# Kernel tuning notes

Measured on AMD Instinct MI355X. Metric: run time of the kernel, lower is better.

Reference implementation:

```python
import jax, jax.numpy as jnp
import numpy as np

M, OUT, IN = 512, 8192, 8192
BLOCK_N, BLOCK_K = 128, 128  # weight_block_size (out_block, in_block)
OB, IB = OUT // BLOCK_N, IN // BLOCK_K  # 64, 64 scale blocks


def setup_inputs() -> dict:
    key = jax.random.key(0)
    k1, k2, k3 = jax.random.split(key, 3)
    x = jax.random.normal(k1, (M, IN), dtype=jnp.float32)
    # pre-quantized int8 weight stored as (out_features, in_features)
    weight_q = jax.random.randint(k2, (OUT, IN), -127, 127, dtype=jnp.int32).astype(jnp.int8)
    # per-(out_block, in_block) dequant scales
    weight_scale = jax.random.uniform(k3, (OB, IB), dtype=jnp.float32, minval=0.01, maxval=0.02)
    return {"x": x, "weight_q": weight_q, "weight_scale": weight_scale}


def _dequant(weight_q, weight_scale):
    # (OUT, IN) int8 -> blocks (OB, BLOCK_N, IB, BLOCK_K), scale broadcast per block
    w = weight_q.astype(jnp.float32).reshape(OB, BLOCK_N, IB, BLOCK_K)
    w = w * weight_scale[:, None, :, None]
    return w.reshape(OUT, IN)


def reference(x, weight_q, weight_scale):
    # Block-dequantize then matmul: out[m, o] = sum_i x[m, i] * (wq[o, i] * scale[o//bn, i//bk])
    w = _dequant(weight_q, weight_scale)          # (OUT, IN) fp32
    out = jnp.einsum("mi,oi->mo", x, w)           # (M, OUT)
    return out
```

## Files before the change

kernel.cpp:

```cpp
#include <hip/hip_runtime.h>

#define MDIM 512
#define NDIM 8192
#define KDIM 8192

typedef float v4f __attribute__((ext_vector_type(4)));
typedef int   v4i __attribute__((ext_vector_type(4)));
typedef char  c16 __attribute__((ext_vector_type(16)));

#define GLDS16(g, l)                                                    \
  __builtin_amdgcn_global_load_lds(                                     \
      (const __attribute__((address_space(1))) void*)(g),               \
      (__attribute__((address_space(3))) void*)(l), 16, 0, 0)
#define SB __builtin_amdgcn_sched_barrier(0)

__device__ __forceinline__ int swb(int row, int g) {
  return ((row >> 1) << 7) + (((((row & 1) << 2) | g) ^ ((row >> 1) & 7)) << 4);
}

__global__ __launch_bounds__(256) void produce_kernel(
    const int* __restrict__ wq, const float* __restrict__ x,
    char* __restrict__ w8, char* __restrict__ xq, float* __restrict__ ax) {
  if (blockIdx.x < 16384) {
    const int tid = blockIdx.x * 256 + threadIdx.x;
    const int R = tid >> 9;
    const int k16 = tid & 511;
    const int* src = wq + ((size_t)R << 13) + k16 * 16;
    v4i a[4];
#pragma unroll
    for (int h = 0; h < 4; ++h) a[h] = *(const v4i*)(src + h * 4);
    c16 q;
#pragma unroll
    for (int h = 0; h < 4; ++h) {
      q[h * 4 + 0] = (char)a[h][0];
      q[h * 4 + 1] = (char)a[h][1];
      q[h * 4 + 2] = (char)a[h][2];
      q[h * 4 + 3] = (char)a[h][3];
    }
    const int ntile = R >> 6, r = R & 63;
    const int kt = k16 >> 2, g = k16 & 3;
    *(c16*)(w8 + ((size_t)(ntile * 128 + kt) << 12) + swb(r, g)) = q;
  } else {
    const int m = blockIdx.x - 16384;
    const int t = threadIdx.x;
    const float* row = x + ((size_t)m << 13);
    v4f v[8];
    float mx = 0.f;
#pragma unroll
    for (int i = 0; i < 8; ++i) {
      v[i] = *(const v4f*)(row + t * 32 + i * 4);
#pragma unroll
      for (int r = 0; r < 4; ++r) mx = fmaxf(mx, fabsf(v[i][r]));
    }
#pragma unroll
    for (int d = 1; d < 64; d <<= 1) mx = fmaxf(mx, __shfl_xor(mx, d));
    __shared__ float smx[4];
    if ((t & 63) == 0) smx[t >> 6] = mx;
    __syncthreads();
    mx = fmaxf(fmaxf(smx[0], smx[1]), fmaxf(smx[2], smx[3]));
    const float inv = (mx > 0.f) ? 127.f / mx : 0.f;
    if (t == 0) ax[m] = mx / 127.f;
    const int mt = m >> 6, r = m & 63;
#pragma unroll
    for (int g2 = 0; g2 < 2; ++g2) {
      c16 q;
#pragma unroll
      for (int e = 0; e < 16; ++e) {
        const int idx = g2 * 4 + (e >> 2);
        float f = fminf(fmaxf(v[idx][e & 3] * inv, -127.f), 127.f);
        q[e] = (char)__float2int_rn(f);
      }
      const int k16 = t * 2 + g2;
      const int kt = k16 >> 2, g = k16 & 3;
      *(c16*)(xq + ((size_t)(mt * 128 + kt) << 12) + swb(r, g)) = q;
    }
  }
}

template <int KS>
__global__ __launch_bounds__(256) void reduce_kernel(const float* __restrict__ p,
                                                     float* __restrict__ out) {
  const size_t i = ((size_t)blockIdx.x * 256 + threadIdx.x) * 4;
  v4f a = *(const v4f*)(p + i);
#pragma unroll
  for (int s = 1; s < KS; ++s) a += *(const v4f*)(p + (size_t)s * MDIM * NDIM + i);
  *(v4f*)(out + i) = a;
}

template <int KS>
__global__ __launch_bounds__(256, 2) void gemm_i8_kernel(
    const char* __restrict__ xq, const char* __restrict__ w8,
    const float* __restrict__ wsc, const float* __restrict__ ax,
    float* __restrict__ outp) {
  constexpr int NPH = 64 / KS;
  __shared__ char lA[2][16384];
  __shared__ char lB[2][16384];

  const int b = blockIdx.x;
  const int c = b & 7;
  const int s = b >> 3;
  const int mt = s & 3;
  const int kh = (KS > 1) ? ((s >> 2) & (KS - 1)) : 0;
  const int nt2 = c * 8 + ((KS > 1) ? (s >> 3) : (s >> 2));
  const int ktg0 = kh * (128 / KS);

  const int t = threadIdx.x;
  const int w = t >> 6, l = t & 63;
  const int wm = (w >> 1) * 64;
  const int wn = (w & 1) * 64;
  const int l15 = l & 15, q = l >> 4;

  v4i acc[4][4] = {};
  v4f facc[4][4] = {};

  auto issue = [&](int tt) {
    const int buf = tt & 1;
#pragma unroll
    for (int it = 0; it < 8; ++it) {
      const int uu = w * 8 + it;
      const int side = uu >> 4;
      const int h = (uu >> 3) & 1;
      const int kt = (uu >> 2) & 1;
      const int qt = uu & 3;
      const int ktile = ktg0 + tt * 2 + kt;
      const char* src =
          (side == 0)
              ? xq + ((size_t)((mt * 2 + h) * 128 + ktile) << 12)
              : w8 + ((size_t)((nt2 * 2 + h) * 128 + ktile) << 12);
      src += qt * 1024 + (size_t)l * 16;
      char* dst = (side == 0) ? &lA[buf][h * 8192 + kt * 4096 + qt * 1024]
                              : &lB[buf][h * 8192 + kt * 4096 + qt * 1024];
      GLDS16(src, dst);
    }
  };

  issue(0);
#pragma unroll 1
  for (int tt = 0; tt < NPH; ++tt) {
    const int cur = tt & 1;
    SB;
    __builtin_amdgcn_s_barrier();
    SB;
    if (tt + 1 < NPH) issue(tt + 1);
    SB;
    if (tt + 1 < NPH)
      asm volatile("s_waitcnt vmcnt(8)" ::: "memory");
    else
      asm volatile("s_waitcnt vmcnt(0)" ::: "memory");
    SB;
    __builtin_amdgcn_s_barrier();
    SB;

#pragma unroll
    for (int kk = 0; kk < 2; ++kk) {
      v4i af[4], bq[4];
#pragma unroll
      for (int i = 0; i < 4; ++i) {
        const int ra = wm + i * 16 + l15;
        af[i] = *(const v4i*)&lA[cur][(ra >> 6) * 8192 + kk * 4096 +
                                      swb(ra & 63, q)];
      }
#pragma unroll
      for (int j = 0; j < 4; ++j) {
        const int rb = wn + j * 16 + l15;
        bq[j] = *(const v4i*)&lB[cur][(rb >> 6) * 8192 + kk * 4096 +
                                      swb(rb & 63, q)];
      }
#pragma unroll
      for (int i = 0; i < 4; ++i)
#pragma unroll
        for (int j = 0; j < 4; ++j)
          acc[i][j] = __builtin_amdgcn_mfma_i32_16x16x64_i8(
              af[i], bq[j], acc[i][j], 0, 0, 0);
    }

    const float sc = wsc[nt2 * 64 + (ktg0 >> 1) + tt];
#pragma unroll
    for (int i = 0; i < 4; ++i)
#pragma unroll
      for (int j = 0; j < 4; ++j) {
#pragma unroll
        for (int r = 0; r < 4; ++r)
          facc[i][j][r] = fmaf(sc, (float)acc[i][j][r], facc[i][j][r]);
        acc[i][j] = v4i{0, 0, 0, 0};
      }
  }

  float* dst = outp + ((KS > 1) ? (size_t)kh * MDIM * NDIM : 0);
#pragma unroll
  for (int i = 0; i < 4; ++i) {
    const int mrow = mt * 128 + wm + i * 16 + q * 4;
#pragma unroll
    for (int j = 0; j < 4; ++j) {
      const int ocol = nt2 * 128 + wn + j * 16 + l15;
#pragma unroll
      for (int r = 0; r < 4; ++r)
        dst[(size_t)(mrow + r) * NDIM + ocol] = ax[mrow + r] * facc[i][j][r];
    }
  }
}

extern "C" void kernel_launch(void* const* d_in, const int* in_sizes, int n_in,
                              void* d_out, int out_size, void* d_ws,
                              size_t ws_size, hipStream_t stream) {
  const float* x = (const float*)d_in[0];
  const int* wq = (const int*)d_in[1];
  const float* wsc = (const float*)d_in[2];
  float* out = (float*)d_out;

  const size_t W8 = (size_t)NDIM * KDIM;
  const size_t XQ = (size_t)MDIM * KDIM;
  const size_t AX = 65536;
  const size_t PS = (size_t)MDIM * NDIM * 4;

  char* w8 = (char*)d_ws;
  char* xq = (char*)d_ws + W8;
  float* ax = (float*)((char*)d_ws + W8 + XQ);
  float* part = (float*)((char*)d_ws + W8 + XQ + AX);

  produce_kernel<<<dim3(16384 + MDIM), dim3(256), 0, stream>>>(wq, x, w8, xq, ax);

  if (ws_size >= W8 + XQ + AX + 2 * PS) {
    gemm_i8_kernel<2><<<dim3(512), dim3(256), 0, stream>>>(xq, w8, wsc, ax, part);
    reduce_kernel<2><<<dim3((MDIM * NDIM) / (256 * 4)), dim3(256), 0, stream>>>(part, out);
  } else {
    gemm_i8_kernel<1><<<dim3(256), dim3(256), 0, stream>>>(xq, w8, wsc, ax, out);
  }
}
```

Measured before the change: 127.7 us.

## Use 512-thread 256x128 GEMM tiles with triple-buffered LDS and split staging

The int8 GEMM now runs 512-thread blocks, each computing a 256x128 output tile. This halves the block count and reuses each staged weight tile across more rows. A three-deep LDS ring of 48 KB stages is refilled in two halves interleaved with each k-subtile's fragment reads, and MFMA sections are raised with s_setprio. The aim is to hide global-to-LDS latency better and cut per-tile weight traffic, at the cost of one block per CU, 144 KB of LDS and an extra barrier per k-tile.

Result: slower. 132.6 us (+3.9%).

```diff
diff --git a/kernel.cpp b/kernel.cpp
--- a/kernel.cpp
+++ b/kernel.cpp
@@ -88,21 +88,20 @@
 }
 
 template <int KS>
-__global__ __launch_bounds__(256, 2) void gemm_i8_kernel(
+__global__ __launch_bounds__(512, 1) void gemm_i8_kernel(
     const char* __restrict__ xq, const char* __restrict__ w8,
     const float* __restrict__ wsc, const float* __restrict__ ax,
     float* __restrict__ outp) {
-  constexpr int NPH = 64 / KS;
-  __shared__ char lA[2][16384];
-  __shared__ char lB[2][16384];
+  constexpr int NKT = 64 / KS;
+  __shared__ char lds[3][49152];
 
   const int b = blockIdx.x;
   const int c = b & 7;
   const int s = b >> 3;
-  const int mt = s & 3;
-  const int kh = (KS > 1) ? ((s >> 2) & (KS - 1)) : 0;
-  const int nt2 = c * 8 + ((KS > 1) ? (s >> 3) : (s >> 2));
-  const int ktg0 = kh * (128 / KS);
+  const int mt = s & 1;
+  const int kh = (s >> 1) & (KS - 1);
+  const int nt = c * 8 + s / (2 * KS);
+  const int k64b = kh * (NKT * 2);
 
   const int t = threadIdx.x;
   const int w = t >> 6, l = t & 63;
@@ -113,68 +112,98 @@
   v4i acc[4][4] = {};
   v4f facc[4][4] = {};
 
-  auto issue = [&](int tt) {
-    const int buf = tt & 1;
-#pragma unroll
-    for (int it = 0; it < 8; ++it) {
-      const int uu = w * 8 + it;
-      const int side = uu >> 4;
-      const int h = (uu >> 3) & 1;
-      const int kt = (uu >> 2) & 1;
-      const int qt = uu & 3;
-      const int ktile = ktg0 + tt * 2 + kt;
-      const char* src =
-          (side == 0)
-              ? xq + ((size_t)((mt * 2 + h) * 128 + ktile) << 12)
-              : w8 + ((size_t)((nt2 * 2 + h) * 128 + ktile) << 12);
-      src += qt * 1024 + (size_t)l * 16;
-      char* dst = (side == 0) ? &lA[buf][h * 8192 + kt * 4096 + qt * 1024]
-                              : &lB[buf][h * 8192 + kt * 4096 + qt * 1024];
-      GLDS16(src, dst);
+  auto stage_half = [&](int t2, int tb, int h) {
+#pragma unroll
+    for (int j = 0; j < 3; ++j) {
+      const int u = h * 24 + w * 3 + j;
+      if (u < 32) {
+        const int sub = u >> 2, qt = u & 3;
+        const int rb = sub >> 1, kt = sub & 1;
+        const char* src =
+            xq + ((size_t)((mt * 4 + rb) * 128 + k64b + t2 * 2 + kt) << 12) +
+            qt * 1024 + (size_t)l * 16;
+        GLDS16(src, &lds[tb][(rb * 2 + kt) * 4096 + qt * 1024]);
+      } else {
+        const int v = u - 32;
+        const int sub = v >> 2, qt = v & 3;
+        const int rb = sub >> 1, kt = sub & 1;
+        const char* src =
+            w8 + ((size_t)((nt * 2 + rb) * 128 + k64b + t2 * 2 + kt) << 12) +
+            qt * 1024 + (size_t)l * 16;
+        GLDS16(src, &lds[tb][32768 + (rb * 2 + kt) * 4096 + qt * 1024]);
+      }
     }
   };
 
-  issue(0);
+  auto read_frags = [&](int cur, int kt, v4i (&af)[4], v4i (&bq)[4]) {
+#pragma unroll
+    for (int i = 0; i < 4; ++i) {
+      const int ra = wm + i * 16 + l15;
+      af[i] = *(const v4i*)&lds[cur][((ra >> 6) * 2 + kt) * 4096 +
+                                     swb(ra & 63, q)];
+    }
+#pragma unroll
+    for (int j = 0; j < 4; ++j) {
+      const int rb = wn + j * 16 + l15;
+      bq[j] = *(const v4i*)&lds[cur][32768 + ((rb >> 6) * 2 + kt) * 4096 +
+                                     swb(rb & 63, q)];
+    }
+  };
+
+  stage_half(0, 0, 0);
+  stage_half(0, 0, 1);
+  stage_half(1, 1, 0);
+  stage_half(1, 1, 1);
+
 #pragma unroll 1
-  for (int tt = 0; tt < NPH; ++tt) {
-    const int cur = tt & 1;
-    SB;
-    __builtin_amdgcn_s_barrier();
-    SB;
-    if (tt + 1 < NPH) issue(tt + 1);
-    SB;
-    if (tt + 1 < NPH)
-      asm volatile("s_waitcnt vmcnt(8)" ::: "memory");
+  for (int tt = 0; tt < NKT; ++tt) {
+    const int cur = tt % 3;
+    const int tgt = (tt + 2) % 3;
+
+    SB;
+    if (tt + 1 < NKT)
+      asm volatile("s_waitcnt vmcnt(6)" ::: "memory");
     else
       asm volatile("s_waitcnt vmcnt(0)" ::: "memory");
     SB;
     __builtin_amdgcn_s_barrier();
     SB;
-
-#pragma unroll
-    for (int kk = 0; kk < 2; ++kk) {
+    {
       v4i af[4], bq[4];
-#pragma unroll
-      for (int i = 0; i < 4; ++i) {
-        const int ra = wm + i * 16 + l15;
-        af[i] = *(const v4i*)&lA[cur][(ra >> 6) * 8192 + kk * 4096 +
-                                      swb(ra & 63, q)];
-      }
-#pragma unroll
-      for (int j = 0; j < 4; ++j) {
-        const int rb = wn + j * 16 + l15;
-        bq[j] = *(const v4i*)&lB[cur][(rb >> 6) * 8192 + kk * 4096 +
-                                      swb(rb & 63, q)];
-      }
+      read_frags(cur, 0, af, bq);
+      if (tt + 2 < NKT) stage_half(tt + 2, tgt, 0);
+      asm volatile("s_waitcnt lgkmcnt(0)" ::: "memory");
+      SB;
+      __builtin_amdgcn_s_setprio(1);
 #pragma unroll
       for (int i = 0; i < 4; ++i)
 #pragma unroll
         for (int j = 0; j < 4; ++j)
-          acc[i][j] = __builtin_amdgcn_mfma_i32_16x16x64_i8(
-              af[i], bq[j], acc[i][j], 0, 0, 0);
-    }
-
-    const float sc = wsc[nt2 * 64 + (ktg0 >> 1) + tt];
+          acc[i][j] = __builtin_amdgcn_mfma_i32_16x16x64_i8(af[i], bq[j],
+                                                            acc[i][j], 0, 0, 0);
+      __builtin_amdgcn_s_setprio(0);
+    }
+
+    SB;
+    __builtin_amdgcn_s_barrier();
+    SB;
+    {
+      v4i af[4], bq[4];
+      read_frags(cur, 1, af, bq);
+      if (tt + 2 < NKT) stage_half(tt + 2, tgt, 1);
+      asm volatile("s_waitcnt lgkmcnt(0)" ::: "memory");
+      SB;
+      __builtin_amdgcn_s_setprio(1);
+#pragma unroll
+      for (int i = 0; i < 4; ++i)
+#pragma unroll
+        for (int j = 0; j < 4; ++j)
+          acc[i][j] = __builtin_amdgcn_mfma_i32_16x16x64_i8(af[i], bq[j],
+                                                            acc[i][j], 0, 0, 0);
+      __builtin_amdgcn_s_setprio(0);
+    }
+
+    const float sc = wsc[nt * 64 + kh * NKT + tt];
 #pragma unroll
     for (int i = 0; i < 4; ++i)
 #pragma unroll
@@ -189,10 +218,10 @@
   float* dst = outp + ((KS > 1) ? (size_t)kh * MDIM * NDIM : 0);
 #pragma unroll
   for (int i = 0; i < 4; ++i) {
-    const int mrow = mt * 128 + wm + i * 16 + q * 4;
+    const int mrow = mt * 256 + wm + i * 16 + q * 4;
 #pragma unroll
     for (int j = 0; j < 4; ++j) {
-      const int ocol = nt2 * 128 + wn + j * 16 + l15;
+      const int ocol = nt * 128 + wn + j * 16 + l15;
 #pragma unroll
       for (int r = 0; r < 4; ++r)
         dst[(size_t)(mrow + r) * NDIM + ocol] = ax[mrow + r] * facc[i][j][r];
@@ -221,9 +250,9 @@
   produce_kernel<<<dim3(16384 + MDIM), dim3(256), 0, stream>>>(wq, x, w8, xq, ax);
 
   if (ws_size >= W8 + XQ + AX + 2 * PS) {
-    gemm_i8_kernel<2><<<dim3(512), dim3(256), 0, stream>>>(xq, w8, wsc, ax, part);
+    gemm_i8_kernel<2><<<dim3(256), dim3(512), 0, stream>>>(xq, w8, wsc, ax, part);
     reduce_kernel<2><<<dim3((MDIM * NDIM) / (256 * 4)), dim3(256), 0, stream>>>(part, out);
   } else {
-    gemm_i8_kernel<1><<<dim3(256), dim3(256), 0, stream>>>(xq, w8, wsc, ax, out);
-  }
-}
+    gemm_i8_kernel<1><<<dim3(128), dim3(512), 0, stream>>>(xq, w8, wsc, ax, out);
+  }
+}
```

## Replace split-K GEMM plus reduce with single-pass 128x64 tile kernel

Applied to the files above, without the earlier changes.

Removes the split-K partial buffers and the separate reduction kernel, so each block computes a 128x64 output tile over the full K range using two waves. This avoids writing and re-reading two full fp32 partial outputs and one kernel launch. In exchange each block has a narrower N tile with less B reuse per A load and fewer waves per block to hide latency.

Measured after the change: 180.7 us. 41.5% more time.

```diff
diff --git a/kernel.cpp b/kernel.cpp
--- a/kernel.cpp
+++ b/kernel.cpp
@@ -77,37 +77,24 @@
   }
 }
 
-template <int KS>
-__global__ __launch_bounds__(256) void reduce_kernel(const float* __restrict__ p,
-                                                     float* __restrict__ out) {
-  const size_t i = ((size_t)blockIdx.x * 256 + threadIdx.x) * 4;
-  v4f a = *(const v4f*)(p + i);
-#pragma unroll
-  for (int s = 1; s < KS; ++s) a += *(const v4f*)(p + (size_t)s * MDIM * NDIM + i);
-  *(v4f*)(out + i) = a;
-}
-
-template <int KS>
-__global__ __launch_bounds__(256, 2) void gemm_i8_kernel(
+__global__ __launch_bounds__(128) void gemm_i8_kernel(
     const char* __restrict__ xq, const char* __restrict__ w8,
     const float* __restrict__ wsc, const float* __restrict__ ax,
-    float* __restrict__ outp) {
-  constexpr int NPH = 64 / KS;
+    float* __restrict__ out) {
+  constexpr int NPH = 64;
   __shared__ char lA[2][16384];
-  __shared__ char lB[2][16384];
+  __shared__ char lB[2][8192];
 
   const int b = blockIdx.x;
   const int c = b & 7;
   const int s = b >> 3;
   const int mt = s & 3;
-  const int kh = (KS > 1) ? ((s >> 2) & (KS - 1)) : 0;
-  const int nt2 = c * 8 + ((KS > 1) ? (s >> 3) : (s >> 2));
-  const int ktg0 = kh * (128 / KS);
+  const int nt = c * 16 + (s >> 2);
+  const int m0 = mt * 128, n0 = nt * 64;
 
   const int t = threadIdx.x;
   const int w = t >> 6, l = t & 63;
-  const int wm = (w >> 1) * 64;
-  const int wn = (w & 1) * 64;
+  const int wm = w * 64;
   const int l15 = l & 15, q = l >> 4;
 
   v4i acc[4][4] = {};
@@ -116,21 +103,22 @@
   auto issue = [&](int tt) {
     const int buf = tt & 1;
 #pragma unroll
-    for (int it = 0; it < 8; ++it) {
-      const int uu = w * 8 + it;
-      const int side = uu >> 4;
-      const int h = (uu >> 3) & 1;
-      const int kt = (uu >> 2) & 1;
-      const int qt = uu & 3;
-      const int ktile = ktg0 + tt * 2 + kt;
-      const char* src =
-          (side == 0)
-              ? xq + ((size_t)((mt * 2 + h) * 128 + ktile) << 12)
-              : w8 + ((size_t)((nt2 * 2 + h) * 128 + ktile) << 12);
-      src += qt * 1024 + (size_t)l * 16;
-      char* dst = (side == 0) ? &lA[buf][h * 8192 + kt * 4096 + qt * 1024]
-                              : &lB[buf][h * 8192 + kt * 4096 + qt * 1024];
-      GLDS16(src, dst);
+    for (int j = 0; j < 12; ++j) {
+      const int u = w * 12 + j;
+      if (u < 16) {
+        const int sub = u >> 2, qt = u & 3;
+        const int h = sub >> 1, kt = sub & 1;
+        const char* src =
+            xq + ((size_t)((mt * 2 + h) * 128 + tt * 2 + kt) << 12) +
+            qt * 1024 + (size_t)l * 16;
+        GLDS16(src, &lA[buf][sub * 4096 + qt * 1024]);
+      } else {
+        const int v = u - 16;
+        const int kt = v >> 2, qt = v & 3;
+        const char* src = w8 + ((size_t)(nt * 128 + tt * 2 + kt) << 12) +
+                          qt * 1024 + (size_t)l * 16;
+        GLDS16(src, &lB[buf][kt * 4096 + qt * 1024]);
+      }
     }
   };
 
@@ -144,7 +132,7 @@
     if (tt + 1 < NPH) issue(tt + 1);
     SB;
     if (tt + 1 < NPH)
-      asm volatile("s_waitcnt vmcnt(8)" ::: "memory");
+      asm volatile("s_waitcnt vmcnt(12)" ::: "memory");
     else
       asm volatile("s_waitcnt vmcnt(0)" ::: "memory");
     SB;
@@ -157,14 +145,13 @@
 #pragma unroll
       for (int i = 0; i < 4; ++i) {
         const int ra = wm + i * 16 + l15;
-        af[i] = *(const v4i*)&lA[cur][(ra >> 6) * 8192 + kk * 4096 +
+        af[i] = *(const v4i*)&lA[cur][((ra >> 6) * 2 + kk) * 4096 +
                                       swb(ra & 63, q)];
       }
 #pragma unroll
       for (int j = 0; j < 4; ++j) {
-        const int rb = wn + j * 16 + l15;
-        bq[j] = *(const v4i*)&lB[cur][(rb >> 6) * 8192 + kk * 4096 +
-                                      swb(rb & 63, q)];
+        const int rb = j * 16 + l15;
+        bq[j] = *(const v4i*)&lB[cur][kk * 4096 + swb(rb, q)];
       }
 #pragma unroll
       for (int i = 0; i < 4; ++i)
@@ -174,7 +161,7 @@
               af[i], bq[j], acc[i][j], 0, 0, 0);
     }
 
-    const float sc = wsc[nt2 * 64 + (ktg0 >> 1) + tt];
+    const float sc = wsc[(nt >> 1) * 64 + tt];
 #pragma unroll
     for (int i = 0; i < 4; ++i)
 #pragma unroll
@@ -186,16 +173,15 @@
       }
   }
 
-  float* dst = outp + ((KS > 1) ? (size_t)kh * MDIM * NDIM : 0);
 #pragma unroll
   for (int i = 0; i < 4; ++i) {
-    const int mrow = mt * 128 + wm + i * 16 + q * 4;
+    const int mrow = m0 + wm + i * 16 + q * 4;
 #pragma unroll
     for (int j = 0; j < 4; ++j) {
-      const int ocol = nt2 * 128 + wn + j * 16 + l15;
+      const int ocol = n0 + j * 16 + l15;
 #pragma unroll
       for (int r = 0; r < 4; ++r)
-        dst[(size_t)(mrow + r) * NDIM + ocol] = ax[mrow + r] * facc[i][j][r];
+        out[(size_t)(mrow + r) * NDIM + ocol] = ax[mrow + r] * facc[i][j][r];
     }
   }
 }
@@ -210,20 +196,11 @@
 
   const size_t W8 = (size_t)NDIM * KDIM;
   const size_t XQ = (size_t)MDIM * KDIM;
-  const size_t AX = 65536;
-  const size_t PS = (size_t)MDIM * NDIM * 4;
 
   char* w8 = (char*)d_ws;
   char* xq = (char*)d_ws + W8;
   float* ax = (float*)((char*)d_ws + W8 + XQ);
-  float* part = (float*)((char*)d_ws + W8 + XQ + AX);
 
   produce_kernel<<<dim3(16384 + MDIM), dim3(256), 0, stream>>>(wq, x, w8, xq, ax);
-
-  if (ws_size >= W8 + XQ + AX + 2 * PS) {
-    gemm_i8_kernel<2><<<dim3(512), dim3(256), 0, stream>>>(xq, w8, wsc, ax, part);
-    reduce_kernel<2><<<dim3((MDIM * NDIM) / (256 * 4)), dim3(256), 0, stream>>>(part, out);
-  } else {
-    gemm_i8_kernel<1><<<dim3(256), dim3(256), 0, stream>>>(xq, w8, wsc, ax, out);
-  }
-}
+  gemm_i8_kernel<<<dim3(512), dim3(128), 0, stream>>>(xq, w8, wsc, ax, out);
+}
```
